# Kernel tuning notes

Measured on AMD Instinct MI355X. Metric: run time of the kernel, lower is better.

The kernel has to match this reference:

```python
import jax, jax.numpy as jnp
import numpy as np

KSZ = 7        # neighborhood kernel size (odd)
HEADS = 16
DIM = 512


def setup_inputs() -> dict:
    key = jax.random.key(0)
    k0, k1, k2, k3 = jax.random.split(key, 4)
    B, C, H, W = 8, DIM, 56, 56
    x = jax.random.normal(k0, (B, C, H, W), jnp.float32)
    qkv_w = jax.random.normal(k1, (3 * C, C), jnp.float32) * 0.02
    rpb = jax.random.normal(k2, (HEADS, 2 * KSZ - 1, 2 * KSZ - 1), jnp.float32) * 0.02
    proj_w = jax.random.normal(k3, (C, C), jnp.float32) * 0.02
    proj_b = jnp.zeros((C,), jnp.float32)
    return {"x": x, "qkv_w": qkv_w, "rpb": rpb, "proj_w": proj_w, "proj_b": proj_b}


def reference(x, qkv_w, rpb, proj_w, proj_b):
    # x: (B, C, H, W) -> NAT forward with dilation=1
    B, C, H, W = x.shape
    h, d = HEADS, C // HEADS
    scale = d ** -0.5
    r = KSZ // 2

    xf = x.transpose(0, 2, 3, 1)                       # (B, H, W, C)
    qkv = (xf @ qkv_w.T).reshape(B, H, W, 3, h, d).transpose(3, 0, 4, 1, 2, 5)
    q, k, v = qkv[0] * scale, qkv[1], qkv[2]           # each (B, h, H, W, d)

    # clamped window starts (NATTEN edge behavior: window shifts, never pads)
    si = jnp.clip(jnp.arange(H) - r, 0, H - KSZ)       # (H,)
    sj = jnp.clip(jnp.arange(W) - r, 0, W - KSZ)       # (W,)
    ii = jnp.arange(H)
    jj = jnp.arange(W)

    # --- QK + relative position bias, looped over the 49 fixed kernel taps ---
    logits = []
    for a in range(KSZ):
        ka = jnp.take(k, si + a, axis=2)               # (B, h, H, W, d)
        bias_i = rpb[:, si + a - ii + (KSZ - 1)]       # (h, H, 2k-1)
        for c in range(KSZ):
            kac = jnp.take(ka, sj + c, axis=3)         # (B, h, H, W, d)
            bj = sj + c - jj + (KSZ - 1)               # (W,)
            l = jnp.einsum('bhijd,bhijd->bhij', q, kac) + bias_i[:, :, bj][None]
            logits.append(l)
    logits = jnp.stack(logits, axis=-1)                # (B, h, H, W, K*K)
    attn = jax.nn.softmax(logits, axis=-1)

    # --- AV gather ---
    out = jnp.zeros_like(q)
    t = 0
    for a in range(KSZ):
        va = jnp.take(v, si + a, axis=2)
        for c in range(KSZ):
            vac = jnp.take(va, sj + c, axis=3)         # (B, h, H, W, d)
            out = out + attn[..., t, None] * vac
            t += 1

    out = out.transpose(0, 2, 3, 1, 4).reshape(B, H, W, C)
    y = out @ proj_w.T + proj_b
    return y.transpose(0, 3, 1, 2)                     # (B, C, H, W)
```

## Files before the change

kernel.cpp:

```cpp
#include <hip/hip_runtime.h>


typedef unsigned short ushort_t;
typedef short bf16x8 __attribute__((ext_vector_type(8)));
typedef short bf16x4 __attribute__((ext_vector_type(4)));
typedef float f32x4 __attribute__((ext_vector_type(4)));
typedef unsigned int uint4_t __attribute__((ext_vector_type(4)));
typedef unsigned int uint2_t __attribute__((ext_vector_type(2)));

#define BATCH 8
#define HEADS 16
#define HW 3136
#define HH 56
#define DD 32
#define CC 512
#define PLANE ((size_t)BATCH * HEADS * HW * DD)
#define OUT_TOT ((size_t)BATCH * CC * HW)
#define LP 40
#define LPG 32

#define KT 14
#define KP 32
#define VPP 228

#define WQ_ELEMS (1536 * 512)
#define WP_ELEMS (512 * 512)

__device__ __forceinline__ ushort_t f2bf(float f) {
    union { float f; unsigned int i; } v; v.f = f;
    unsigned int r = v.i + 0x7FFFu + ((v.i >> 16) & 1u);
    return (ushort_t)(r >> 16);
}
__device__ __forceinline__ unsigned int pack2(float a, float b) {
    return (unsigned int)f2bf(a) | ((unsigned int)f2bf(b) << 16);
}

__device__ __forceinline__ f32x4 mfma16x16x16(bf16x4 a, bf16x4 b, f32x4 c) {
#if __has_builtin(__builtin_amdgcn_mfma_f32_16x16x16bf16_1k)
    return __builtin_amdgcn_mfma_f32_16x16x16bf16_1k(a, b, c, 0, 0, 0);
#else
    f32x4 d;
    asm("v_mfma_f32_16x16x16_bf16 %0, %1, %2, %3" : "=v"(d) : "v"(a), "v"(b), "v"(c));
    return d;
#endif
}

__device__ __forceinline__ void gload16(const ushort_t* g, ushort_t* l) {
    __builtin_amdgcn_global_load_lds(
        (const __attribute__((address_space(1))) unsigned int*)g,
        (__attribute__((address_space(3))) unsigned int*)l, 16, 0, 0);
}

__global__ __launch_bounds__(256) void zero_out_f32(float* __restrict__ out) {
    size_t idx = (size_t)blockIdx.x * 256 + threadIdx.x;
    if (idx < OUT_TOT) out[idx] = 0.f;
}

__global__ __launch_bounds__(256) void cvt_f32_bf16(const float* __restrict__ src,
                                                    ushort_t* __restrict__ dst, int n8) {
    int idx = blockIdx.x * 256 + threadIdx.x;
    if (idx >= n8) return;
    const float4* s = (const float4*)src + (size_t)idx * 2;
    float4 f0 = s[0], f1 = s[1];
    uint4_t u;
    u[0] = pack2(f0.x, f0.y);
    u[1] = pack2(f0.z, f0.w);
    u[2] = pack2(f1.x, f1.y);
    u[3] = pack2(f1.z, f1.w);
    *(uint4_t*)(dst + (size_t)idx * 8) = u;
}

__global__ __launch_bounds__(256) void xpose_cvt(const float* __restrict__ x,
                                                 ushort_t* __restrict__ xb) {
    __shared__ ushort_t T[64 * 64];
    int tid = threadIdx.x;
    int hw0 = blockIdx.x * 64;
    int c0 = blockIdx.y * 64;
    int b = blockIdx.z;

    int cr = tid >> 2, hq = tid & 3;
    const float* src = x + ((size_t)b * CC + c0 + cr) * HW + hw0 + hq * 16;
    float4 f0 = *(const float4*)(src);
    float4 f1 = *(const float4*)(src + 4);
    float4 f2 = *(const float4*)(src + 8);
    float4 f3 = *(const float4*)(src + 12);
    uint4_t u0, u1;
    u0[0] = pack2(f0.x, f0.y); u0[1] = pack2(f0.z, f0.w);
    u0[2] = pack2(f1.x, f1.y); u0[3] = pack2(f1.z, f1.w);
    u1[0] = pack2(f2.x, f2.y); u1[1] = pack2(f2.z, f2.w);
    u1[2] = pack2(f3.x, f3.y); u1[3] = pack2(f3.z, f3.w);
    int sw = ((cr >> 4) & 3) << 4;
    int col0 = (hq * 16) ^ sw;
    *(uint4_t*)&T[cr * 64 + col0] = u0;
    *(uint4_t*)&T[cr * 64 + col0 + 8] = u1;

    __syncthreads();

    int p = tid >> 2, cq = tid & 3;
    int pc = p ^ (cq << 4);
    unsigned vv[8];
    #pragma unroll
    for (int j = 0; j < 16; j += 2) {
        unsigned a = T[(cq * 16 + j) * 64 + pc];
        unsigned b2 = T[(cq * 16 + j + 1) * 64 + pc];
        vv[j >> 1] = a | (b2 << 16);
    }
    ushort_t* dst = xb + ((size_t)b * HW + hw0 + p) * CC + c0 + cq * 16;
    uint4_t w0, w1;
    w0[0] = vv[0]; w0[1] = vv[1]; w0[2] = vv[2]; w0[3] = vv[3];
    w1[0] = vv[4]; w1[1] = vv[5]; w1[2] = vv[6]; w1[3] = vv[7];
    *(uint4_t*)&dst[0] = w0;
    *(uint4_t*)&dst[8] = w1;
}

__global__ __launch_bounds__(256) void qkv_gemm_bf16(const ushort_t* __restrict__ xb,
                                                     const ushort_t* __restrict__ w,
                                                     ushort_t* __restrict__ qkv) {
    __shared__ __align__(16) ushort_t lds_p[2][256 * LPG];
    __shared__ __align__(16) ushort_t lds_q[2][64 * LPG];
    int tid = threadIdx.x;
    int b = blockIdx.z;
    int n0 = blockIdx.y * 256;
    int p0 = blockIdx.x * 64;
    int lane = tid & 63, wv = tid >> 6;
    int wp = wv & 1, wq = wv >> 1;
    int quad = lane >> 4, l15 = lane & 15;

    f32x4 acc[8][2];
    #pragma unroll
    for (int i = 0; i < 8; ++i)
        #pragma unroll
        for (int jq = 0; jq < 2; ++jq) acc[i][jq] = (f32x4){0.f, 0.f, 0.f, 0.f};

    int swz = (l15 >> 1) & 3;
    int cha = (quad ^ swz) * 8;

    int ca_row[4], ca_k8[4];
    #pragma unroll
    for (int r = 0; r < 4; ++r) {
        int c = r * 256 + tid;
        ca_row[r] = c >> 2;
        ca_k8[r] = ((c & 3) ^ ((c >> 3) & 3)) * 8;
    }
    int cb_row = tid >> 2;
    int cb_k8 = ((tid & 3) ^ ((tid >> 3) & 3)) * 8;

    const int NKT = CC / 32;
    #pragma unroll
    for (int r = 0; r < 4; ++r)
        gload16(w + (size_t)(n0 + ca_row[r]) * CC + ca_k8[r], &lds_p[0][(r * 256 + tid) * 8]);
    gload16(xb + ((size_t)b * HW + p0 + cb_row) * CC + cb_k8, &lds_q[0][tid * 8]);
    __syncthreads();

    for (int kt = 0; kt < NKT; ++kt) {
        int cur = kt & 1;
        if (kt + 1 < NKT) {
            int ko = (kt + 1) * 32;
            #pragma unroll
            for (int r = 0; r < 4; ++r)
                gload16(w + (size_t)(n0 + ca_row[r]) * CC + ko + ca_k8[r],
                        &lds_p[cur ^ 1][(r * 256 + tid) * 8]);
            gload16(xb + ((size_t)b * HW + p0 + cb_row) * CC + ko + cb_k8,
                    &lds_q[cur ^ 1][tid * 8]);
        }
        bf16x8 afrag[8], bfrag[2];
        #pragma unroll
        for (int i = 0; i < 8; ++i)
            afrag[i] = *(const bf16x8*)&lds_p[cur][(wp * 128 + i * 16 + l15) * LPG + cha];
        #pragma unroll
        for (int jq = 0; jq < 2; ++jq)
            bfrag[jq] = *(const bf16x8*)&lds_q[cur][(wq * 32 + jq * 16 + l15) * LPG + cha];
        #pragma unroll
        for (int i = 0; i < 8; ++i)
            #pragma unroll
            for (int jq = 0; jq < 2; ++jq)
                acc[i][jq] = __builtin_amdgcn_mfma_f32_16x16x32_bf16(afrag[i], bfrag[jq],
                                                                     acc[i][jq], 0, 0, 0);
        __syncthreads();
    }
    const float qscale = 0.17677669529663687f;
    #pragma unroll
    for (int i = 0; i < 8; ++i) {
        int nbase = n0 + wp * 128 + i * 16 + quad * 4;
        int which = nbase >> 9;
        int h = (nbase >> 5) & 15;
        int dch = nbase & 31;
        float sc = (which == 0) ? qscale : 1.0f;
        #pragma unroll
        for (int jq = 0; jq < 2; ++jq) {
            int pix = p0 + wq * 32 + jq * 16 + l15;
            uint2_t v;
            v[0] = pack2(acc[i][jq][0] * sc, acc[i][jq][1] * sc);
            v[1] = pack2(acc[i][jq][2] * sc, acc[i][jq][3] * sc);
            ushort_t* dst = qkv + (size_t)which * PLANE +
                            ((((size_t)b * HEADS + h) * HW + pix) * DD + dch);
            *(uint2_t*)dst = v;
        }
    }
}

__global__ __launch_bounds__(256) void qkv_gemm_kernel(const float* __restrict__ x,
                                                       const float* __restrict__ w,
                                                       ushort_t* __restrict__ qkv) {
    __shared__ __align__(16) ushort_t lds_p[128 * LP];
    __shared__ __align__(16) ushort_t lds_q[64 * LP];
    const int K = CC;
    int tid = threadIdx.x;
    int b = blockIdx.z;
    int n0 = blockIdx.y * 128;
    int p0 = blockIdx.x * 64;
    int lane = tid & 63, wv = tid >> 6;
    int wp = wv & 1, wq = wv >> 1;
    int quad = lane >> 4, l15 = lane & 15;

    f32x4 acc[4][2];
    #pragma unroll
    for (int i = 0; i < 4; ++i)
        #pragma unroll
        for (int jq = 0; jq < 2; ++jq) acc[i][jq] = (f32x4){0.f, 0.f, 0.f, 0.f};

    int spx = tid & 63;
    int sk8 = (tid >> 6) * 8;

    for (int kt = 0; kt < K / 32; ++kt) {
        __syncthreads();
        #pragma unroll
        for (int r = 0; r < 2; ++r) {
            int chunk = tid + r * 256;
            int row = chunk >> 2, k8 = (chunk & 3) * 8;
            const float* src = w + (size_t)(n0 + row) * K + kt * 32 + k8;
            float4 f0 = *(const float4*)src;
            float4 f1 = *(const float4*)(src + 4);
            uint4_t u;
            u[0] = pack2(f0.x, f0.y);
            u[1] = pack2(f0.z, f0.w);
            u[2] = pack2(f1.x, f1.y);
            u[3] = pack2(f1.z, f1.w);
            *(uint4_t*)&lds_p[row * LP + k8] = u;
        }
        {
            const float* xcol = x + ((size_t)b * CC + kt * 32 + sk8) * HW + p0 + spx;
            float v0 = xcol[0];
            float v1 = xcol[(size_t)HW];
            float v2 = xcol[(size_t)2 * HW];
            float v3 = xcol[(size_t)3 * HW];
            float v4 = xcol[(size_t)4 * HW];
            float v5 = xcol[(size_t)5 * HW];
            float v6 = xcol[(size_t)6 * HW];
            float v7 = xcol[(size_t)7 * HW];
            uint4_t u;
            u[0] = pack2(v0, v1);
            u[1] = pack2(v2, v3);
            u[2] = pack2(v4, v5);
            u[3] = pack2(v6, v7);
            *(uint4_t*)&lds_q[spx * LP + sk8] = u;
        }
        __syncthreads();
        bf16x8 afrag[4], bfrag[2];
        #pragma unroll
        for (int i = 0; i < 4; ++i)
            afrag[i] = *(const bf16x8*)&lds_p[(wp * 64 + i * 16 + l15) * LP + quad * 8];
        #pragma unroll
        for (int jq = 0; jq < 2; ++jq)
            bfrag[jq] = *(const bf16x8*)&lds_q[(wq * 32 + jq * 16 + l15) * LP + quad * 8];
        #pragma unroll
        for (int i = 0; i < 4; ++i)
            #pragma unroll
            for (int jq = 0; jq < 2; ++jq)
                acc[i][jq] = __builtin_amdgcn_mfma_f32_16x16x32_bf16(afrag[i], bfrag[jq],
                                                                     acc[i][jq], 0, 0, 0);
    }
    const float qscale = 0.17677669529663687f;
    #pragma unroll
    for (int i = 0; i < 4; ++i) {
        int nbase = n0 + wp * 64 + i * 16 + quad * 4;
        int which = nbase >> 9;
        int h = (nbase >> 5) & 15;
        int dch = nbase & 31;
        float sc = (which == 0) ? qscale : 1.0f;
        #pragma unroll
        for (int jq = 0; jq < 2; ++jq) {
            int pix = p0 + wq * 32 + jq * 16 + l15;
            uint2_t v;
            v[0] = pack2(acc[i][jq][0] * sc, acc[i][jq][1] * sc);
            v[1] = pack2(acc[i][jq][2] * sc, acc[i][jq][3] * sc);
            ushort_t* dst = qkv + (size_t)which * PLANE +
                            ((((size_t)b * HEADS + h) * HW + pix) * DD + dch);
            *(uint2_t*)dst = v;
        }
    }
}

__global__ __launch_bounds__(256, 4) void attn_mfma(ushort_t* __restrict__ qkv,
                                                    const float* __restrict__ rpb) {
    __shared__ __align__(16) ushort_t Klds[224 * KP];
    __shared__ __align__(16) ushort_t Vlds[DD * VPP];
    __shared__ float rpbl[169];

    int tid = threadIdx.x;
    int b = blockIdx.z, h = blockIdx.y;
    int tile = blockIdx.x;
    int ti = tile / 7, tj = tile - ti * 7;
    int i0 = ti * 8, j0 = tj * 8;
    int kr0 = min(max(i0 - 3, 0), HH - 14);
    int kc0 = min(max(j0 - 3, 0), HH - 14);

    const ushort_t* qp = qkv + (((size_t)b * HEADS + h) * HW) * DD;
    const ushort_t* kp = qp + PLANE;
    const ushort_t* vp = qp + 2 * PLANE;

    if (tid < 169) rpbl[tid] = rpb[h * 169 + tid];

    #pragma unroll
    for (int r = 0; r < 4; ++r) {
        int idx = tid + r * 256;
        if (idx < 784) {
            int u = idx / 56;
            int rem = idx - u * 56;
            int w = rem >> 2, d8 = (rem & 3) << 3;
            const ushort_t* src = kp + ((size_t)((kr0 + u) * HH + kc0 + w)) * DD + d8;
            *(uint4_t*)&Klds[(u * 16 + w) * KP + d8] = *(const uint4_t*)src;
        } else if (idx < 896) {
            int z = idx - 784;
            int u = z >> 3, rem = z & 7;
            int w = 14 + (rem >> 2), d8 = (rem & 3) << 3;
            *(uint4_t*)&Klds[(u * 16 + w) * KP + d8] = (uint4_t){0, 0, 0, 0};
        }
    }
    #pragma unroll
    for (int rr = 0; rr < 2; ++rr) {
        int idx = tid + rr * 256;
        if (idx < 448) {
            int u = idx >> 5, rem = idx & 31;
            int pr = rem >> 2, d8 = (rem & 3) << 3;
            int kk0 = u * 16 + pr * 2;
            if (pr < 7) {
                const ushort_t* s0 = vp + ((size_t)((kr0 + u) * HH + kc0 + pr * 2)) * DD + d8;
                uint4_t a = *(const uint4_t*)s0;
                uint4_t c = *(const uint4_t*)(s0 + DD);
                #pragma unroll
                for (int e = 0; e < 4; ++e) {
                    unsigned lo = (a[e] & 0xFFFFu) | (c[e] << 16);
                    unsigned hi = (a[e] >> 16) | (c[e] & 0xFFFF0000u);
                    *(unsigned*)&Vlds[(d8 + 2 * e) * VPP + kk0] = lo;
                    *(unsigned*)&Vlds[(d8 + 2 * e + 1) * VPP + kk0] = hi;
                }
            } else {
                #pragma unroll
                for (int e = 0; e < 8; ++e)
                    *(unsigned*)&Vlds[(d8 + e) * VPP + kk0] = 0;
            }
        }
    }

    int lane = tid & 63, wv = tid >> 6;
    int l15 = lane & 15, quad = lane >> 4;
    int q_idx = wv * 16 + l15;
    int qi = i0 + (q_idx >> 3), qj = j0 + (q_idx & 7);
    int si = min(max(qi - 3, 0), HH - 7);
    int sj = min(max(qj - 3, 0), HH - 7);

    bf16x8 bq = *(const bf16x8*)(qp + ((size_t)(qi * HH + qj)) * DD + quad * 8);

    int jbase = kc0 + quad * 4 - sj;
    int cbase = kc0 + quad * 4 - qj + 6;
    int coff[4];
    bool cok[4];
    #pragma unroll
    for (int r2 = 0; r2 < 4; ++r2) {
        cok[r2] = (unsigned)(jbase + r2) <= 6u;
        coff[r2] = min(max(cbase + r2, 0), 12);
    }

    __syncthreads();

    f32x4 lg[KT];
    f32x4 zf = {0.f, 0.f, 0.f, 0.f};
    #pragma unroll
    for (int t = 0; t < KT; ++t) {
        bf16x8 ak = *(const bf16x8*)&Klds[(t * 16 + l15) * KP + quad * 8];
        lg[t] = __builtin_amdgcn_mfma_f32_16x16x32_bf16(ak, bq, zf, 0, 0, 0);
    }

    int abase = kr0 - qi + 6;
    #pragma unroll
    for (int t = 0; t < KT; ++t) {
        bool rok = (unsigned)(kr0 + t - si) <= 6u;
        int arow = min(max(abase + t, 0), 12);
        const float* br = &rpbl[arow * 13];
        #pragma unroll
        for (int r2 = 0; r2 < 4; ++r2) {
            float bias = br[coff[r2]];
            lg[t][r2] = (rok && cok[r2]) ? lg[t][r2] + bias : -1e30f;
        }
    }

    float m = -1e30f;
    #pragma unroll
    for (int t = 0; t < KT; ++t)
        #pragma unroll
        for (int r2 = 0; r2 < 4; ++r2) m = fmaxf(m, lg[t][r2]);
    m = fmaxf(m, __shfl_xor(m, 16));
    m = fmaxf(m, __shfl_xor(m, 32));
    float s = 0.f;
    #pragma unroll
    for (int t = 0; t < KT; ++t)
        #pragma unroll
        for (int r2 = 0; r2 < 4; ++r2) {
            float e = __expf(lg[t][r2] - m);
            lg[t][r2] = e;
            s += e;
        }
    s += __shfl_xor(s, 16);
    s += __shfl_xor(s, 32);
    float inv = 1.f / s;

    bf16x4 pb[KT];
    #pragma unroll
    for (int t = 0; t < KT; ++t) {
        union { uint2_t u; bf16x4 v; } cv;
        cv.u[0] = pack2(lg[t][0], lg[t][1]);
        cv.u[1] = pack2(lg[t][2], lg[t][3]);
        pb[t] = cv.v;
    }

    f32x4 acc0 = zf, acc1 = zf;
    #pragma unroll
    for (int t = 0; t < KT; ++t) {
        bf16x4 bv0 = *(const bf16x4*)&Vlds[l15 * VPP + t * 16 + quad * 4];
        bf16x4 bv1 = *(const bf16x4*)&Vlds[(16 + l15) * VPP + t * 16 + quad * 4];
        acc0 = mfma16x16x16(pb[t], bv0, acc0);
        acc1 = mfma16x16x16(pb[t], bv1, acc1);
    }

    ushort_t* op = qkv + (((size_t)b * HEADS + h) * HW) * DD;
    #pragma unroll
    for (int e = 0; e < 4; ++e) {
        float invq = __shfl(inv, quad * 4 + e);
        int q2 = wv * 16 + quad * 4 + e;
        int pix = (i0 + (q2 >> 3)) * HH + j0 + (q2 & 7);
        op[(size_t)pix * DD + l15] = f2bf(acc0[e] * invq);
        op[(size_t)pix * DD + 16 + l15] = f2bf(acc1[e] * invq);
    }
}

__global__ __launch_bounds__(256) void proj_gemm_bf16(const ushort_t* __restrict__ ao,
                                                      const ushort_t* __restrict__ w,
                                                      const float* __restrict__ bias,
                                                      float* __restrict__ out) {
    __shared__ __align__(16) ushort_t lds_p[2][64 * LPG];
    __shared__ __align__(16) ushort_t lds_q[2][128 * LPG];
    int tid = threadIdx.x;
    int b = blockIdx.z;
    int p0 = blockIdx.x * 64;
    int c0 = blockIdx.y * 128;
    int lane = tid & 63, wv = tid >> 6;
    int wp = wv & 1, wq = wv >> 1;
    int quad = lane >> 4, l15 = lane & 15;

    f32x4 acc[2][4];
    #pragma unroll
    for (int i = 0; i < 2; ++i)
        #pragma unroll
        for (int jq = 0; jq < 4; ++jq) acc[i][jq] = (f32x4){0.f, 0.f, 0.f, 0.f};

    const ushort_t* abase = ao + ((size_t)b * HEADS) * HW * DD;
    int swz = (l15 >> 1) & 3;
    int cha = (quad ^ swz) * 8;

    int ca_row = tid >> 2;
    int ca_k8 = ((tid & 3) ^ ((tid >> 3) & 3)) * 8;
    int cb_row[2], cb_k8[2];
    #pragma unroll
    for (int r = 0; r < 2; ++r) {
        int c = r * 256 + tid;
        cb_row[r] = c >> 2;
        cb_k8[r] = ((c & 3) ^ ((c >> 3) & 3)) * 8;
    }

    const int NKT = CC / 32;
    gload16(abase + ((size_t)0 * HW + p0 + ca_row) * DD + ca_k8, &lds_p[0][tid * 8]);
    #pragma unroll
    for (int r = 0; r < 2; ++r)
        gload16(w + (size_t)(c0 + cb_row[r]) * CC + cb_k8[r],
                &lds_q[0][(r * 256 + tid) * 8]);
    __syncthreads();

    for (int kt = 0; kt < NKT; ++kt) {
        int cur = kt & 1;
        if (kt + 1 < NKT) {
            int kn = kt + 1;
            gload16(abase + ((size_t)kn * HW + p0 + ca_row) * DD + ca_k8,
                    &lds_p[cur ^ 1][tid * 8]);
            #pragma unroll
            for (int r = 0; r < 2; ++r)
                gload16(w + (size_t)(c0 + cb_row[r]) * CC + kn * 32 + cb_k8[r],
                        &lds_q[cur ^ 1][(r * 256 + tid) * 8]);
        }
        bf16x8 afrag[2], bfrag[4];
        #pragma unroll
        for (int i = 0; i < 2; ++i)
            afrag[i] = *(const bf16x8*)&lds_p[cur][(wp * 32 + i * 16 + l15) * LPG + cha];
        #pragma unroll
        for (int jq = 0; jq < 4; ++jq)
            bfrag[jq] = *(const bf16x8*)&lds_q[cur][(wq * 64 + jq * 16 + l15) * LPG + cha];
        #pragma unroll
        for (int i = 0; i < 2; ++i)
            #pragma unroll
            for (int jq = 0; jq < 4; ++jq)
                acc[i][jq] = __builtin_amdgcn_mfma_f32_16x16x32_bf16(afrag[i], bfrag[jq],
                                                                     acc[i][jq], 0, 0, 0);
        __syncthreads();
    }
    #pragma unroll
    for (int i = 0; i < 2; ++i) {
        int pix = p0 + wp * 32 + i * 16 + quad * 4;
        #pragma unroll
        for (int jq = 0; jq < 4; ++jq) {
            int cch = c0 + wq * 64 + jq * 16 + l15;
            float bz = bias[cch];
            float4 v;
            v.x = acc[i][jq][0] + bz;
            v.y = acc[i][jq][1] + bz;
            v.z = acc[i][jq][2] + bz;
            v.w = acc[i][jq][3] + bz;
            float* dst = out + ((size_t)b * CC + cch) * HW + pix;
            *(float4*)dst = v;
        }
    }
}

__global__ __launch_bounds__(256) void proj_gemm_kernel(const ushort_t* __restrict__ ao,
                                                        const float* __restrict__ w,
                                                        const float* __restrict__ bias,
                                                        float* __restrict__ out) {
    __shared__ __align__(16) ushort_t lds_p[64 * LP];
    __shared__ __align__(16) ushort_t lds_q[128 * LP];
    const int K = CC;
    int tid = threadIdx.x;
    int b = blockIdx.z;
    int p0 = blockIdx.x * 64;
    int c0 = blockIdx.y * 128;
    int lane = tid & 63, wv = tid >> 6;
    int wp = wv & 1, wq = wv >> 1;
    int quad = lane >> 4, l15 = lane & 15;

    f32x4 acc[2][4];
    #pragma unroll
    for (int i = 0; i < 2; ++i)
        #pragma unroll
        for (int jq = 0; jq < 4; ++jq) acc[i][jq] = (f32x4){0.f, 0.f, 0.f, 0.f};

    const ushort_t* abase = ao + ((size_t)b * HEADS) * HW * DD;

    for (int kt = 0; kt < K / 32; ++kt) {
        __syncthreads();
        {
            int row = tid >> 2, k8 = (tid & 3) * 8;
            uint4_t u = *(const uint4_t*)(abase + ((size_t)kt * HW + p0 + row) * DD + k8);
            *(uint4_t*)&lds_p[row * LP + k8] = u;
        }
        #pragma unroll
        for (int r = 0; r < 2; ++r) {
            int chunk = tid + r * 256;
            int row = chunk >> 2, k8 = (chunk & 3) * 8;
            const float* src = w + (size_t)(c0 + row) * K + kt * 32 + k8;
            float4 f0 = *(const float4*)src;
            float4 f1 = *(const float4*)(src + 4);
            uint4_t u;
            u[0] = pack2(f0.x, f0.y);
            u[1] = pack2(f0.z, f0.w);
            u[2] = pack2(f1.x, f1.y);
            u[3] = pack2(f1.z, f1.w);
            *(uint4_t*)&lds_q[row * LP + k8] = u;
        }
        __syncthreads();
        bf16x8 afrag[2], bfrag[4];
        #pragma unroll
        for (int i = 0; i < 2; ++i)
            afrag[i] = *(const bf16x8*)&lds_p[(wp * 32 + i * 16 + l15) * LP + quad * 8];
        #pragma unroll
        for (int jq = 0; jq < 4; ++jq)
            bfrag[jq] = *(const bf16x8*)&lds_q[(wq * 64 + jq * 16 + l15) * LP + quad * 8];
        #pragma unroll
        for (int i = 0; i < 2; ++i)
            #pragma unroll
            for (int jq = 0; jq < 4; ++jq)
                acc[i][jq] = __builtin_amdgcn_mfma_f32_16x16x32_bf16(afrag[i], bfrag[jq],
                                                                     acc[i][jq], 0, 0, 0);
    }
    #pragma unroll
    for (int i = 0; i < 2; ++i) {
        int pix = p0 + wp * 32 + i * 16 + quad * 4;
        #pragma unroll
        for (int jq = 0; jq < 4; ++jq) {
            int cch = c0 + wq * 64 + jq * 16 + l15;
            float bz = bias[cch];
            float4 v;
            v.x = acc[i][jq][0] + bz;
            v.y = acc[i][jq][1] + bz;
            v.z = acc[i][jq][2] + bz;
            v.w = acc[i][jq][3] + bz;
            float* dst = out + ((size_t)b * CC + cch) * HW + pix;
            *(float4*)dst = v;
        }
    }
}

extern "C" void kernel_launch(void* const* d_in, const int* in_sizes, int n_in,
                              void* d_out, int out_size, void* d_ws, size_t ws_size,
                              hipStream_t stream) {
    const float* x = (const float*)d_in[0];
    const float* qkv_w = (const float*)d_in[1];
    const float* rpb = (const float*)d_in[2];
    const float* proj_w = (const float*)d_in[3];
    const float* proj_b = (const float*)d_in[4];
    float* out = (float*)d_out;

    size_t need_min = 3 * PLANE * sizeof(ushort_t);
    size_t need_full = (4 * PLANE + WQ_ELEMS + WP_ELEMS) * sizeof(ushort_t);

    if (ws_size < need_min) {
        zero_out_f32<<<dim3((int)((OUT_TOT + 255) / 256)), dim3(256), 0, stream>>>(out);
        return;
    }

    ushort_t* qkv = (ushort_t*)d_ws;

    if (ws_size >= need_full) {
        ushort_t* xbf = qkv + 3 * PLANE;
        ushort_t* wqb = qkv + 4 * PLANE;
        ushort_t* wpb = wqb + WQ_ELEMS;

        xpose_cvt<<<dim3(49, 8, 8), dim3(256), 0, stream>>>(x, xbf);
        cvt_f32_bf16<<<dim3((WQ_ELEMS / 8 + 255) / 256), dim3(256), 0, stream>>>(
            qkv_w, wqb, WQ_ELEMS / 8);
        cvt_f32_bf16<<<dim3((WP_ELEMS / 8 + 255) / 256), dim3(256), 0, stream>>>(
            proj_w, wpb, WP_ELEMS / 8);

        qkv_gemm_bf16<<<dim3(49, 6, 8), dim3(256), 0, stream>>>(xbf, wqb, qkv);
        attn_mfma<<<dim3(49, HEADS, BATCH), dim3(256), 0, stream>>>(qkv, rpb);
        proj_gemm_bf16<<<dim3(49, 4, 8), dim3(256), 0, stream>>>(qkv, wpb, proj_b, out);
    } else {
        qkv_gemm_kernel<<<dim3(49, 12, 8), dim3(256), 0, stream>>>(x, qkv_w, qkv);
        attn_mfma<<<dim3(49, HEADS, BATCH), dim3(256), 0, stream>>>(qkv, rpb);
        proj_gemm_kernel<<<dim3(49, 4, 8), dim3(256), 0, stream>>>(qkv, proj_w, proj_b, out);
    }
}
```

Before: 255.2 us.

## Shrink QKV GEMM tile, merge weight conversions, raise MFMA priority in attention

The QKV GEMM tile is halved along the output-channel dimension (256 to 128 rows), doubling the grid to 12 column blocks per batch. This gives more blocks and fewer accumulator registers per thread, which may help occupancy and balance across CUs at the cost of reloading the activation tile more often. The two weight-conversion launches are merged into a single kernel to save launch overhead. In the attention kernel, s_setprio is raised around the MFMA loops so MFMA-issuing waves get scheduling priority.

```diff
diff --git a/kernel.cpp b/kernel.cpp
--- a/kernel.cpp
+++ b/kernel.cpp
@@ -56,18 +56,29 @@
     if (idx < OUT_TOT) out[idx] = 0.f;
 }
 
-__global__ __launch_bounds__(256) void cvt_f32_bf16(const float* __restrict__ src,
-                                                    ushort_t* __restrict__ dst, int n8) {
+__global__ __launch_bounds__(256) void cvt_weights(const float* __restrict__ wa,
+                                                   ushort_t* __restrict__ da, int n8a,
+                                                   const float* __restrict__ wb,
+                                                   ushort_t* __restrict__ db, int n8b) {
     int idx = blockIdx.x * 256 + threadIdx.x;
-    if (idx >= n8) return;
-    const float4* s = (const float4*)src + (size_t)idx * 2;
-    float4 f0 = s[0], f1 = s[1];
+    const float* s;
+    ushort_t* d;
+    int i;
+    if (idx < n8a) {
+        s = wa; d = da; i = idx;
+    } else {
+        i = idx - n8a;
+        if (i >= n8b) return;
+        s = wb; d = db;
+    }
+    const float4* sp = (const float4*)s + (size_t)i * 2;
+    float4 f0 = sp[0], f1 = sp[1];
     uint4_t u;
     u[0] = pack2(f0.x, f0.y);
     u[1] = pack2(f0.z, f0.w);
     u[2] = pack2(f1.x, f1.y);
     u[3] = pack2(f1.z, f1.w);
-    *(uint4_t*)(dst + (size_t)idx * 8) = u;
+    *(uint4_t*)(d + (size_t)i * 8) = u;
 }
 
 __global__ __launch_bounds__(256) void xpose_cvt(const float* __restrict__ x,
@@ -116,28 +127,28 @@
 __global__ __launch_bounds__(256) void qkv_gemm_bf16(const ushort_t* __restrict__ xb,
                                                      const ushort_t* __restrict__ w,
                                                      ushort_t* __restrict__ qkv) {
-    __shared__ __align__(16) ushort_t lds_p[2][256 * LPG];
+    __shared__ __align__(16) ushort_t lds_p[2][128 * LPG];
     __shared__ __align__(16) ushort_t lds_q[2][64 * LPG];
     int tid = threadIdx.x;
     int b = blockIdx.z;
-    int n0 = blockIdx.y * 256;
+    int n0 = blockIdx.y * 128;
     int p0 = blockIdx.x * 64;
     int lane = tid & 63, wv = tid >> 6;
     int wp = wv & 1, wq = wv >> 1;
     int quad = lane >> 4, l15 = lane & 15;
 
-    f32x4 acc[8][2];
-    #pragma unroll
-    for (int i = 0; i < 8; ++i)
+    f32x4 acc[4][2];
+    #pragma unroll
+    for (int i = 0; i < 4; ++i)
         #pragma unroll
         for (int jq = 0; jq < 2; ++jq) acc[i][jq] = (f32x4){0.f, 0.f, 0.f, 0.f};
 
     int swz = (l15 >> 1) & 3;
     int cha = (quad ^ swz) * 8;
 
-    int ca_row[4], ca_k8[4];
-    #pragma unroll
-    for (int r = 0; r < 4; ++r) {
+    int ca_row[2], ca_k8[2];
+    #pragma unroll
+    for (int r = 0; r < 2; ++r) {
         int c = r * 256 + tid;
         ca_row[r] = c >> 2;
         ca_k8[r] = ((c & 3) ^ ((c >> 3) & 3)) * 8;
@@ -147,8 +158,9 @@
 
     const int NKT = CC / 32;
     #pragma unroll
-    for (int r = 0; r < 4; ++r)
-        gload16(w + (size_t)(n0 + ca_row[r]) * CC + ca_k8[r], &lds_p[0][(r * 256 + tid) * 8]);
+    for (int r = 0; r < 2; ++r)
+        gload16(w + (size_t)(n0 + ca_row[r]) * CC + ca_k8[r],
+                &lds_p[0][(r * 256 + tid) * 8]);
     gload16(xb + ((size_t)b * HW + p0 + cb_row) * CC + cb_k8, &lds_q[0][tid * 8]);
     __syncthreads();
 
@@ -157,21 +169,21 @@
         if (kt + 1 < NKT) {
             int ko = (kt + 1) * 32;
             #pragma unroll
-            for (int r = 0; r < 4; ++r)
+            for (int r = 0; r < 2; ++r)
                 gload16(w + (size_t)(n0 + ca_row[r]) * CC + ko + ca_k8[r],
                         &lds_p[cur ^ 1][(r * 256 + tid) * 8]);
             gload16(xb + ((size_t)b * HW + p0 + cb_row) * CC + ko + cb_k8,
                     &lds_q[cur ^ 1][tid * 8]);
         }
-        bf16x8 afrag[8], bfrag[2];
-        #pragma unroll
-        for (int i = 0; i < 8; ++i)
-            afrag[i] = *(const bf16x8*)&lds_p[cur][(wp * 128 + i * 16 + l15) * LPG + cha];
+        bf16x8 afrag[4], bfrag[2];
+        #pragma unroll
+        for (int i = 0; i < 4; ++i)
+            afrag[i] = *(const bf16x8*)&lds_p[cur][(wp * 64 + i * 16 + l15) * LPG + cha];
         #pragma unroll
         for (int jq = 0; jq < 2; ++jq)
             bfrag[jq] = *(const bf16x8*)&lds_q[cur][(wq * 32 + jq * 16 + l15) * LPG + cha];
         #pragma unroll
-        for (int i = 0; i < 8; ++i)
+        for (int i = 0; i < 4; ++i)
             #pragma unroll
             for (int jq = 0; jq < 2; ++jq)
                 acc[i][jq] = __builtin_amdgcn_mfma_f32_16x16x32_bf16(afrag[i], bfrag[jq],
@@ -180,8 +192,8 @@
     }
     const float qscale = 0.17677669529663687f;
     #pragma unroll
-    for (int i = 0; i < 8; ++i) {
-        int nbase = n0 + wp * 128 + i * 16 + quad * 4;
+    for (int i = 0; i < 4; ++i) {
+        int nbase = n0 + wp * 64 + i * 16 + quad * 4;
         int which = nbase >> 9;
         int h = (nbase >> 5) & 15;
         int dch = nbase & 31;
@@ -376,11 +388,13 @@
 
     f32x4 lg[KT];
     f32x4 zf = {0.f, 0.f, 0.f, 0.f};
+    __builtin_amdgcn_s_setprio(1);
     #pragma unroll
     for (int t = 0; t < KT; ++t) {
         bf16x8 ak = *(const bf16x8*)&Klds[(t * 16 + l15) * KP + quad * 8];
         lg[t] = __builtin_amdgcn_mfma_f32_16x16x32_bf16(ak, bq, zf, 0, 0, 0);
     }
+    __builtin_amdgcn_s_setprio(0);
 
     int abase = kr0 - qi + 6;
     #pragma unroll
@@ -425,6 +439,7 @@
     }
 
     f32x4 acc0 = zf, acc1 = zf;
+    __builtin_amdgcn_s_setprio(1);
     #pragma unroll
     for (int t = 0; t < KT; ++t) {
         bf16x4 bv0 = *(const bf16x4*)&Vlds[l15 * VPP + t * 16 + quad * 4];
@@ -432,6 +447,7 @@
         acc0 = mfma16x16x16(pb[t], bv0, acc0);
         acc1 = mfma16x16x16(pb[t], bv1, acc1);
     }
+    __builtin_amdgcn_s_setprio(0);
 
     ushort_t* op = qkv + (((size_t)b * HEADS + h) * HW) * DD;
     #pragma unroll
@@ -633,12 +649,10 @@
         ushort_t* wpb = wqb + WQ_ELEMS;
 
         xpose_cvt<<<dim3(49, 8, 8), dim3(256), 0, stream>>>(x, xbf);
-        cvt_f32_bf16<<<dim3((WQ_ELEMS / 8 + 255) / 256), dim3(256), 0, stream>>>(
-            qkv_w, wqb, WQ_ELEMS / 8);
-        cvt_f32_bf16<<<dim3((WP_ELEMS / 8 + 255) / 256), dim3(256), 0, stream>>>(
-            proj_w, wpb, WP_ELEMS / 8);
-
-        qkv_gemm_bf16<<<dim3(49, 6, 8), dim3(256), 0, stream>>>(xbf, wqb, qkv);
+        cvt_weights<<<dim3((WQ_ELEMS / 8 + WP_ELEMS / 8 + 255) / 256), dim3(256), 0,
+                      stream>>>(qkv_w, wqb, WQ_ELEMS / 8, proj_w, wpb, WP_ELEMS / 8);
+
+        qkv_gemm_bf16<<<dim3(49, 12, 8), dim3(256), 0, stream>>>(xbf, wqb, qkv);
         attn_mfma<<<dim3(49, HEADS, BATCH), dim3(256), 0, stream>>>(qkv, rpb);
         proj_gemm_bf16<<<dim3(49, 4, 8), dim3(256), 0, stream>>>(qkv, wpb, proj_b, out);
     } else {
```

Result: slower. 268.5 us (+5.2%).
